# Kernel tuning notes

Hardware: AMD Instinct MI355X
Metric: run time of the kernel (lower is better)

The kernel has to match this reference:

```python
import jax, jax.numpy as jnp
import numpy as np

B, N, C = 64, 1700, 256
E_SP, E_TM = 6400, 10000


def gcn_conv(x, W, b, edge_index, num_nodes):
    """PyG GCNConv (normalize=True, add_self_loops=True) on batched [B,N,C] input,
    gathering/scattering along the node axis (node_dim=-2)."""
    row, col = edge_index[0], edge_index[1]
    loops = jnp.arange(num_nodes, dtype=row.dtype)
    row = jnp.concatenate([row, loops])
    col = jnp.concatenate([col, loops])
    w = jnp.ones(row.shape[0], dtype=x.dtype)
    deg = jax.ops.segment_sum(w, col, num_segments=num_nodes)
    dinv = jnp.where(deg > 0, jax.lax.rsqrt(deg), jnp.zeros_like(deg))
    norm = dinv[row] * dinv[col]                      # [E+N]
    h = x @ W                                         # [B,N,Cout]
    msg = h[:, row, :] * norm[None, :, None]          # gather along joints
    out = jnp.zeros((x.shape[0], num_nodes, W.shape[1]), x.dtype)
    out = out.at[:, col, :].add(msg)                  # scatter-add along joints
    return out + b


def setup_inputs() -> dict:
    key = jax.random.key(0)
    ks = jax.random.split(key, 9)
    s = 1.0 / np.sqrt(C)
    return {
        "x": jax.random.normal(ks[0], (B, N, C), jnp.float32),
        "W1": jax.random.uniform(ks[1], (C, C), jnp.float32, -s, s),
        "b1": jnp.zeros((C,), jnp.float32),
        "W2": jax.random.uniform(ks[2], (C, C), jnp.float32, -s, s),
        "b2": jnp.zeros((C,), jnp.float32),
        "W3": jax.random.uniform(ks[3], (C, C), jnp.float32, -s, s),
        "b3": jnp.zeros((C,), jnp.float32),
        "keypoint_line_without_temporal": jax.random.randint(ks[4], (2, E_SP), 0, N, jnp.int32),
        "keypoint_line_with_temporal": jax.random.randint(ks[5], (2, E_TM), 0, N, jnp.int32),
    }


def reference(x, W1, b1, W2, b2, W3, b3,
              keypoint_line_without_temporal, keypoint_line_with_temporal):
    num_nodes = x.shape[1]
    residual = x  # downsample is None -> identity residual
    out = jax.nn.relu(gcn_conv(x, W1, b1, keypoint_line_without_temporal, num_nodes))
    out = jax.nn.relu(gcn_conv(out, W2, b2, keypoint_line_with_temporal, num_nodes))
    out = gcn_conv(out, W3, b3, keypoint_line_without_temporal, num_nodes)
    return jax.nn.relu(out + residual)
```

## Files before the change

### kernel.cpp

```cpp
#include <hip/hip_runtime.h>

#define NNODES 1700
#define CDIM   256

typedef __attribute__((ext_vector_type(8))) short bf16x8;
typedef __attribute__((ext_vector_type(4))) float f32x4;

__device__ inline float bf2f(unsigned h) { return __uint_as_float(h << 16); }
__device__ inline unsigned short f2bf(float f) {
  unsigned u = __float_as_uint(f);
  u = (u + 0x7FFFu + ((u >> 16) & 1u)) >> 16;
  return (unsigned short)u;
}

__device__ inline void async_copy16(const void* gsrc, void* ldst) {
  __builtin_amdgcn_global_load_lds(
      (const __attribute__((address_space(1))) unsigned int*)gsrc,
      (__attribute__((address_space(3))) unsigned int*)ldst,
      16, 0, 0);
}


__global__ __launch_bounds__(256) void prep1(const float* __restrict__ W1,
                                             const float* __restrict__ W2,
                                             const float* __restrict__ W3,
                                             unsigned short* __restrict__ Wt,
                                             int* __restrict__ zb) {
  int i = blockIdx.x * 256 + threadIdx.x;
  if (i < 4 * NNODES) zb[i] = 0;
  if (i < 3 * 65536) {
    int wsel = i >> 16, e = i & 65535;
    const float* W = wsel == 0 ? W1 : (wsel == 1 ? W2 : W3);
    int k = e >> 8, n = e & 255;
    Wt[(wsel << 16) + n * 256 + k] = f2bf(W[e]);
  }
}

__global__ __launch_bounds__(256) void prep2(const int* __restrict__ esp, int Esp,
                                             const int* __restrict__ etm, int Etm,
                                             int* __restrict__ cnt_sp,
                                             int* __restrict__ cnt_tm) {
  int i = blockIdx.x * 256 + threadIdx.x;
  if (i < Esp) {
    atomicAdd(&cnt_sp[esp[Esp + i]], 1);
  } else {
    int k = i - Esp;
    if (k < Etm) atomicAdd(&cnt_tm[etm[Etm + k]], 1);
  }
}

__global__ __launch_bounds__(1024) void prep3(const int* __restrict__ cnt_sp,
                                              float* __restrict__ dinv_sp,
                                              int* __restrict__ off_sp,
                                              const int* __restrict__ cnt_tm,
                                              float* __restrict__ dinv_tm,
                                              int* __restrict__ off_tm) {
  const int* cnt = blockIdx.x ? cnt_tm : cnt_sp;
  float* dinv = blockIdx.x ? dinv_tm : dinv_sp;
  int* off = blockIdx.x ? off_tm : off_sp;
  __shared__ int s[2048];
  int t = threadIdx.x;
  for (int i = t; i < NNODES; i += 1024) dinv[i] = rsqrtf((float)(cnt[i] + 1));
  for (int i = t; i < 2048; i += 1024) s[i] = (i < NNODES) ? (cnt[i] + 1) : 0;
  for (int d = 1; d < 2048; d <<= 1) {
    __syncthreads();
    int idx = (t + 1) * (d << 1) - 1;
    if (idx < 2048) s[idx] += s[idx - d];
  }
  __syncthreads();
  if (t == 0) s[2047] = 0;
  for (int d = 1024; d >= 1; d >>= 1) {
    __syncthreads();
    int idx = (t + 1) * (d << 1) - 1;
    if (idx < 2048) { int tmp = s[idx - d]; s[idx - d] = s[idx]; s[idx] += tmp; }
  }
  __syncthreads();
  for (int i = t; i <= NNODES; i += 1024) off[i] = s[i];
}

__global__ __launch_bounds__(256) void prep4(
    const int* __restrict__ esp, int Esp, const int* __restrict__ etm, int Etm,
    const float* __restrict__ dinv_sp, const int* __restrict__ off_sp,
    int* __restrict__ cur_sp, int* __restrict__ src_sp, float* __restrict__ wgt_sp,
    const float* __restrict__ dinv_tm, const int* __restrict__ off_tm,
    int* __restrict__ cur_tm, int* __restrict__ src_tm, float* __restrict__ wgt_tm) {
  int i = blockIdx.x * 256 + threadIdx.x;
  const int tot_sp = Esp + NNODES;
  if (i < tot_sp) {
    int s, d;
    if (i < Esp) { s = esp[i]; d = esp[Esp + i]; } else { s = d = i - Esp; }
    float w = dinv_sp[s] * dinv_sp[d];
    int p = atomicAdd(&cur_sp[d], 1);
    int idx = off_sp[d] + p;
    src_sp[idx] = s; wgt_sp[idx] = w;
  } else {
    int k = i - tot_sp;
    if (k < Etm + NNODES) {
      int s, d;
      if (k < Etm) { s = etm[k]; d = etm[Etm + k]; } else { s = d = k - Etm; }
      float w = dinv_tm[s] * dinv_tm[d];
      int p = atomicAdd(&cur_tm[d], 1);
      int idx = off_tm[d] + p;
      src_tm[idx] = s; wgt_tm[idx] = w;
    }
  }
}


template <bool SRCF32>
__global__ __launch_bounds__(256) void agg_kernel(const void* __restrict__ Xp,
                                                  const int* __restrict__ off,
                                                  const int* __restrict__ srcv,
                                                  const float* __restrict__ wv,
                                                  unsigned short* __restrict__ Xa) {
  const int n = blockIdx.x;
  const int b = blockIdx.y * 8 + (threadIdx.x >> 5);
  const int c = (threadIdx.x & 31) * 8;
  const int beg = off[n], end = off[n + 1];
  const size_t base = (size_t)b * NNODES;

  float a0 = 0.f, a1 = 0.f, a2 = 0.f, a3 = 0.f;
  float a4 = 0.f, a5 = 0.f, a6 = 0.f, a7 = 0.f;
  for (int i = beg; i < end; i += 2) {
    int s0 = srcv[i];
    float w0 = wv[i];
    const bool two = (i + 1 < end);
    int i1 = two ? i + 1 : i;
    int s1 = srcv[i1];
    float w1 = two ? wv[i1] : 0.f;
    if (SRCF32) {
      const float* X = (const float*)Xp;
      const float* p0 = X + (base + s0) * CDIM + c;
      const float* p1 = X + (base + s1) * CDIM + c;
      float4 u0 = *(const float4*)p0, u1 = *(const float4*)(p0 + 4);
      float4 v0 = *(const float4*)p1, v1 = *(const float4*)(p1 + 4);
      a0 += w0 * u0.x + w1 * v0.x; a1 += w0 * u0.y + w1 * v0.y;
      a2 += w0 * u0.z + w1 * v0.z; a3 += w0 * u0.w + w1 * v0.w;
      a4 += w0 * u1.x + w1 * v1.x; a5 += w0 * u1.y + w1 * v1.y;
      a6 += w0 * u1.z + w1 * v1.z; a7 += w0 * u1.w + w1 * v1.w;
    } else {
      const unsigned short* X = (const unsigned short*)Xp;
      uint4 u = *(const uint4*)(X + (base + s0) * CDIM + c);
      uint4 v = *(const uint4*)(X + (base + s1) * CDIM + c);
      a0 += w0 * bf2f(u.x & 0xffffu) + w1 * bf2f(v.x & 0xffffu);
      a1 += w0 * bf2f(u.x >> 16)     + w1 * bf2f(v.x >> 16);
      a2 += w0 * bf2f(u.y & 0xffffu) + w1 * bf2f(v.y & 0xffffu);
      a3 += w0 * bf2f(u.y >> 16)     + w1 * bf2f(v.y >> 16);
      a4 += w0 * bf2f(u.z & 0xffffu) + w1 * bf2f(v.z & 0xffffu);
      a5 += w0 * bf2f(u.z >> 16)     + w1 * bf2f(v.z >> 16);
      a6 += w0 * bf2f(u.w & 0xffffu) + w1 * bf2f(v.w & 0xffffu);
      a7 += w0 * bf2f(u.w >> 16)     + w1 * bf2f(v.w >> 16);
    }
  }
  bf16x8 ov;
  ov[0] = (short)f2bf(a0); ov[1] = (short)f2bf(a1);
  ov[2] = (short)f2bf(a2); ov[3] = (short)f2bf(a3);
  ov[4] = (short)f2bf(a4); ov[5] = (short)f2bf(a5);
  ov[6] = (short)f2bf(a6); ov[7] = (short)f2bf(a7);
  *(bf16x8*)(Xa + (base + n) * CDIM + c) = ov;
}


template <int K>
__device__ __forceinline__ void kstep(const unsigned short* __restrict__ asrc,
                                      const unsigned short* __restrict__ bsrc,
                                      unsigned short (&As)[2][128 * 32],
                                      unsigned short (&Bs)[2][64 * 32],
                                      int t, int wm, int wn, int lr, int lk,
                                      f32x4 (&acc)[4][2]) {
  if constexpr (K < 7) {
    asm volatile("s_waitcnt vmcnt(3)" ::: "memory");
  } else {
    asm volatile("s_waitcnt vmcnt(0)" ::: "memory");
  }
  __builtin_amdgcn_s_barrier();
  bf16x8 a[4], b[2];
#pragma unroll
  for (int i = 0; i < 4; i++)
    a[i] = *(const bf16x8*)&As[K & 1][(wm + i * 16 + lr) * 32 + lk];
#pragma unroll
  for (int i = 0; i < 2; i++)
    b[i] = *(const bf16x8*)&Bs[K & 1][(wn + i * 16 + lr) * 32 + lk];
  asm volatile("s_waitcnt lgkmcnt(0)" ::: "memory");
  __builtin_amdgcn_sched_barrier(0);
  __builtin_amdgcn_s_barrier();
  if constexpr (K + 2 < 8) {
    constexpr int S = K + 2;
    async_copy16(asrc + S * 32, &As[S & 1][t * 8]);
    async_copy16(asrc + (size_t)64 * CDIM + S * 32, &As[S & 1][2048 + t * 8]);
    async_copy16(bsrc + S * 32, &Bs[S & 1][t * 8]);
  }
#pragma unroll
  for (int mi = 0; mi < 4; mi++)
#pragma unroll
    for (int ni = 0; ni < 2; ni++)
      acc[mi][ni] = __builtin_amdgcn_mfma_f32_16x16x32_bf16(a[mi], b[ni], acc[mi][ni], 0, 0, 0);
}

template <bool FINAL>
__global__ __launch_bounds__(256, 5) void gemm_t64(const unsigned short* __restrict__ A,
                                                   const unsigned short* __restrict__ Wt,
                                                   const float* __restrict__ bias,
                                                   const float* __restrict__ resid,
                                                   void* __restrict__ outp) {
  __shared__ __align__(16) unsigned short As[2][128 * 32];
  __shared__ __align__(16) unsigned short Bs[2][64 * 32];
  const int t = threadIdx.x;
  const int lane = t & 63;
  const int w = t >> 6;
  const int wm = (w & 1) * 64;
  const int wn = (w >> 1) * 32;
  const int lr = lane & 15;
  const int lk = (lane >> 4) * 8;

  const int chunk = gridDim.x >> 3;
  const int swz = (blockIdx.x & 7) * chunk + (blockIdx.x >> 3);
  const int m0 = (swz >> 2) * 128;
  const int n0 = (swz & 3) * 64;

  const unsigned short* asrc = A + (size_t)(m0 + (t >> 2)) * CDIM + (t & 3) * 8;
  const unsigned short* bsrc = Wt + (size_t)(n0 + (t >> 2)) * CDIM + (t & 3) * 8;

  f32x4 acc[4][2] = {};

#pragma unroll
  for (int s = 0; s < 2; s++) {
    async_copy16(asrc + s * 32, &As[s][t * 8]);
    async_copy16(asrc + (size_t)64 * CDIM + s * 32, &As[s][2048 + t * 8]);
    async_copy16(bsrc + s * 32, &Bs[s][t * 8]);
  }

  kstep<0>(asrc, bsrc, As, Bs, t, wm, wn, lr, lk, acc);
  kstep<1>(asrc, bsrc, As, Bs, t, wm, wn, lr, lk, acc);
  kstep<2>(asrc, bsrc, As, Bs, t, wm, wn, lr, lk, acc);
  kstep<3>(asrc, bsrc, As, Bs, t, wm, wn, lr, lk, acc);
  kstep<4>(asrc, bsrc, As, Bs, t, wm, wn, lr, lk, acc);
  kstep<5>(asrc, bsrc, As, Bs, t, wm, wn, lr, lk, acc);
  kstep<6>(asrc, bsrc, As, Bs, t, wm, wn, lr, lk, acc);
  kstep<7>(asrc, bsrc, As, Bs, t, wm, wn, lr, lk, acc);

  float bv[2];
#pragma unroll
  for (int ni = 0; ni < 2; ni++) bv[ni] = bias[n0 + wn + ni * 16 + lr];
  const int orow = (lane >> 4) * 4;
#pragma unroll
  for (int mi = 0; mi < 4; mi++) {
#pragma unroll
    for (int ni = 0; ni < 2; ni++) {
#pragma unroll
      for (int r = 0; r < 4; r++) {
        const size_t gr = (size_t)(m0 + wm + mi * 16 + orow + r);
        const size_t idx = gr * CDIM + n0 + wn + ni * 16 + lr;
        float v = acc[mi][ni][r] + bv[ni];
        if (FINAL) {
          v += resid[idx];
          ((float*)outp)[idx] = fmaxf(v, 0.f);
        } else {
          ((unsigned short*)outp)[idx] = f2bf(fmaxf(v, 0.f));
        }
      }
    }
  }
}


extern "C" void kernel_launch(void* const* d_in, const int* in_sizes, int n_in,
                              void* d_out, int out_size, void* d_ws, size_t ws_size,
                              hipStream_t stream) {
  const float* x  = (const float*)d_in[0];
  const float* W1 = (const float*)d_in[1];
  const float* b1 = (const float*)d_in[2];
  const float* W2 = (const float*)d_in[3];
  const float* b2 = (const float*)d_in[4];
  const float* W3 = (const float*)d_in[5];
  const float* b3 = (const float*)d_in[6];
  const int* esp = (const int*)d_in[7];
  const int* etm = (const int*)d_in[8];

  const int Esp = in_sizes[7] / 2;
  const int Etm = in_sizes[8] / 2;
  const int B = in_sizes[0] / (NNODES * CDIM);
  const int M = B * NNODES;

  char* ws = (char*)d_ws;
  size_t woff = 0;
  auto alloc = [&](size_t bytes) -> void* {
    void* p = ws + woff;
    woff = (woff + bytes + 255) & ~(size_t)255;
    return p;
  };

  unsigned short* H   = (unsigned short*)alloc((size_t)M * CDIM * 2);
  unsigned short* Act = (unsigned short*)alloc((size_t)M * CDIM * 2);
  unsigned short* Wt  = (unsigned short*)alloc((size_t)3 * CDIM * CDIM * 2);
  int* zero_base = (int*)alloc((size_t)4 * NNODES * sizeof(int));
  int* cnt_sp = zero_base;
  int* cur_sp = zero_base + NNODES;
  int* cnt_tm = zero_base + 2 * NNODES;
  int* cur_tm = zero_base + 3 * NNODES;
  int* off_sp = (int*)alloc((NNODES + 1) * sizeof(int));
  int* off_tm = (int*)alloc((NNODES + 1) * sizeof(int));
  float* dinv_sp = (float*)alloc(NNODES * sizeof(float));
  float* dinv_tm = (float*)alloc(NNODES * sizeof(float));
  int*   src_sp = (int*)alloc((size_t)(Esp + NNODES) * sizeof(int));
  float* wgt_sp = (float*)alloc((size_t)(Esp + NNODES) * sizeof(float));
  int*   src_tm = (int*)alloc((size_t)(Etm + NNODES) * sizeof(int));
  float* wgt_tm = (float*)alloc((size_t)(Etm + NNODES) * sizeof(float));

  prep1<<<(3 * 65536 + 255) / 256, 256, 0, stream>>>(W1, W2, W3, Wt, zero_base);
  prep2<<<(Esp + Etm + 255) / 256, 256, 0, stream>>>(esp, Esp, etm, Etm, cnt_sp, cnt_tm);
  prep3<<<2, 1024, 0, stream>>>(cnt_sp, dinv_sp, off_sp, cnt_tm, dinv_tm, off_tm);
  prep4<<<(Esp + Etm + 2 * NNODES + 255) / 256, 256, 0, stream>>>(
      esp, Esp, etm, Etm, dinv_sp, off_sp, cur_sp, src_sp, wgt_sp,
      dinv_tm, off_tm, cur_tm, src_tm, wgt_tm);

  dim3 agrid(NNODES, B / 8);
  dim3 ggrid(4 * (M / 128));

  agg_kernel<true><<<agrid, 256, 0, stream>>>(x, off_sp, src_sp, wgt_sp, Act);
  gemm_t64<false><<<ggrid, 256, 0, stream>>>(Act, Wt, b1, nullptr, H);
  agg_kernel<false><<<agrid, 256, 0, stream>>>(H, off_tm, src_tm, wgt_tm, Act);
  gemm_t64<false><<<ggrid, 256, 0, stream>>>(Act, Wt + CDIM * CDIM, b2, nullptr, H);
  agg_kernel<false><<<agrid, 256, 0, stream>>>(H, off_sp, src_sp, wgt_sp, Act);
  gemm_t64<true><<<ggrid, 256, 0, stream>>>(Act, Wt + 2 * CDIM * CDIM, b3, x, d_out);
}
```

Before: 437.5 us.

## Split aggregation into per-dtype kernels with finer thread mapping; stage GEMM stores through LDS

The aggregation kernel is split into f32 and bf16 variants where each thread handles 4 channels instead of 8. Blocks cover fewer batches (2 or 4) and use a swizzled 1D grid, which raises parallelism and memory-level concurrency for the gather-heavy step. The non-final GEMM epilogue now stages bf16 results in shared memory and writes 16-byte coalesced rows instead of scattered 2-byte stores. The costs are more blocks, more index loads per byte fetched, and extra barriers in the epilogue.

After: 420.9 us. -3.8%, faster.

```diff
diff --git a/kernel.cpp b/kernel.cpp
--- a/kernel.cpp
+++ b/kernel.cpp
@@ -107,20 +107,21 @@
 }
 
 
-template <bool SRCF32>
-__global__ __launch_bounds__(256) void agg_kernel(const void* __restrict__ Xp,
-                                                  const int* __restrict__ off,
-                                                  const int* __restrict__ srcv,
-                                                  const float* __restrict__ wv,
-                                                  unsigned short* __restrict__ Xa) {
-  const int n = blockIdx.x;
-  const int b = blockIdx.y * 8 + (threadIdx.x >> 5);
-  const int c = (threadIdx.x & 31) * 8;
+__global__ __launch_bounds__(128) void agg_f32(const float* __restrict__ X,
+                                               const int* __restrict__ off,
+                                               const int* __restrict__ srcv,
+                                               const float* __restrict__ wv,
+                                               unsigned short* __restrict__ Xa) {
+  const int perx = gridDim.x >> 3;
+  const int gidx = (blockIdx.x & 7) * perx + (blockIdx.x >> 3);
+  const int g = gidx / NNODES;
+  const int n = gidx - g * NNODES;
+  const int b = g * 2 + (threadIdx.x >> 6);
+  const int c = (threadIdx.x & 63) * 4;
   const int beg = off[n], end = off[n + 1];
   const size_t base = (size_t)b * NNODES;
 
   float a0 = 0.f, a1 = 0.f, a2 = 0.f, a3 = 0.f;
-  float a4 = 0.f, a5 = 0.f, a6 = 0.f, a7 = 0.f;
   for (int i = beg; i < end; i += 2) {
     int s0 = srcv[i];
     float w0 = wv[i];
@@ -128,44 +129,57 @@
     int i1 = two ? i + 1 : i;
     int s1 = srcv[i1];
     float w1 = two ? wv[i1] : 0.f;
-    if (SRCF32) {
-      const float* X = (const float*)Xp;
-      const float* p0 = X + (base + s0) * CDIM + c;
-      const float* p1 = X + (base + s1) * CDIM + c;
-      float4 u0 = *(const float4*)p0, u1 = *(const float4*)(p0 + 4);
-      float4 v0 = *(const float4*)p1, v1 = *(const float4*)(p1 + 4);
-      a0 += w0 * u0.x + w1 * v0.x; a1 += w0 * u0.y + w1 * v0.y;
-      a2 += w0 * u0.z + w1 * v0.z; a3 += w0 * u0.w + w1 * v0.w;
-      a4 += w0 * u1.x + w1 * v1.x; a5 += w0 * u1.y + w1 * v1.y;
-      a6 += w0 * u1.z + w1 * v1.z; a7 += w0 * u1.w + w1 * v1.w;
-    } else {
-      const unsigned short* X = (const unsigned short*)Xp;
-      uint4 u = *(const uint4*)(X + (base + s0) * CDIM + c);
-      uint4 v = *(const uint4*)(X + (base + s1) * CDIM + c);
-      a0 += w0 * bf2f(u.x & 0xffffu) + w1 * bf2f(v.x & 0xffffu);
-      a1 += w0 * bf2f(u.x >> 16)     + w1 * bf2f(v.x >> 16);
-      a2 += w0 * bf2f(u.y & 0xffffu) + w1 * bf2f(v.y & 0xffffu);
-      a3 += w0 * bf2f(u.y >> 16)     + w1 * bf2f(v.y >> 16);
-      a4 += w0 * bf2f(u.z & 0xffffu) + w1 * bf2f(v.z & 0xffffu);
-      a5 += w0 * bf2f(u.z >> 16)     + w1 * bf2f(v.z >> 16);
-      a6 += w0 * bf2f(u.w & 0xffffu) + w1 * bf2f(v.w & 0xffffu);
-      a7 += w0 * bf2f(u.w >> 16)     + w1 * bf2f(v.w >> 16);
-    }
-  }
-  bf16x8 ov;
-  ov[0] = (short)f2bf(a0); ov[1] = (short)f2bf(a1);
-  ov[2] = (short)f2bf(a2); ov[3] = (short)f2bf(a3);
-  ov[4] = (short)f2bf(a4); ov[5] = (short)f2bf(a5);
-  ov[6] = (short)f2bf(a6); ov[7] = (short)f2bf(a7);
-  *(bf16x8*)(Xa + (base + n) * CDIM + c) = ov;
+    float4 u = *(const float4*)(X + (base + s0) * CDIM + c);
+    float4 v = *(const float4*)(X + (base + s1) * CDIM + c);
+    a0 += w0 * u.x + w1 * v.x; a1 += w0 * u.y + w1 * v.y;
+    a2 += w0 * u.z + w1 * v.z; a3 += w0 * u.w + w1 * v.w;
+  }
+  uint2 o;
+  o.x = (unsigned)f2bf(a0) | ((unsigned)f2bf(a1) << 16);
+  o.y = (unsigned)f2bf(a2) | ((unsigned)f2bf(a3) << 16);
+  *(uint2*)(Xa + (base + n) * CDIM + c) = o;
+}
+
+__global__ __launch_bounds__(256) void agg_bf16(const unsigned short* __restrict__ X,
+                                                const int* __restrict__ off,
+                                                const int* __restrict__ srcv,
+                                                const float* __restrict__ wv,
+                                                unsigned short* __restrict__ Xa) {
+  const int perx = gridDim.x >> 3;
+  const int gidx = (blockIdx.x & 7) * perx + (blockIdx.x >> 3);
+  const int g = gidx / NNODES;
+  const int n = gidx - g * NNODES;
+  const int b = g * 4 + (threadIdx.x >> 6);
+  const int c = (threadIdx.x & 63) * 4;
+  const int beg = off[n], end = off[n + 1];
+  const size_t base = (size_t)b * NNODES;
+
+  float a0 = 0.f, a1 = 0.f, a2 = 0.f, a3 = 0.f;
+  for (int i = beg; i < end; i += 2) {
+    int s0 = srcv[i];
+    float w0 = wv[i];
+    const bool two = (i + 1 < end);
+    int i1 = two ? i + 1 : i;
+    int s1 = srcv[i1];
+    float w1 = two ? wv[i1] : 0.f;
+    uint2 u = *(const uint2*)(X + (base + s0) * CDIM + c);
+    uint2 v = *(const uint2*)(X + (base + s1) * CDIM + c);
+    a0 += w0 * bf2f(u.x & 0xffffu) + w1 * bf2f(v.x & 0xffffu);
+    a1 += w0 * bf2f(u.x >> 16)     + w1 * bf2f(v.x >> 16);
+    a2 += w0 * bf2f(u.y & 0xffffu) + w1 * bf2f(v.y & 0xffffu);
+    a3 += w0 * bf2f(u.y >> 16)     + w1 * bf2f(v.y >> 16);
+  }
+  uint2 o;
+  o.x = (unsigned)f2bf(a0) | ((unsigned)f2bf(a1) << 16);
+  o.y = (unsigned)f2bf(a2) | ((unsigned)f2bf(a3) << 16);
+  *(uint2*)(Xa + (base + n) * CDIM + c) = o;
 }
 
 
 template <int K>
 __device__ __forceinline__ void kstep(const unsigned short* __restrict__ asrc,
                                       const unsigned short* __restrict__ bsrc,
-                                      unsigned short (&As)[2][128 * 32],
-                                      unsigned short (&Bs)[2][64 * 32],
+                                      unsigned short* SH,
                                       int t, int wm, int wn, int lr, int lk,
                                       f32x4 (&acc)[4][2]) {
   if constexpr (K < 7) {
@@ -177,18 +191,18 @@
   bf16x8 a[4], b[2];
 #pragma unroll
   for (int i = 0; i < 4; i++)
-    a[i] = *(const bf16x8*)&As[K & 1][(wm + i * 16 + lr) * 32 + lk];
+    a[i] = *(const bf16x8*)&SH[(K & 1) * 4096 + (wm + i * 16 + lr) * 32 + lk];
 #pragma unroll
   for (int i = 0; i < 2; i++)
-    b[i] = *(const bf16x8*)&Bs[K & 1][(wn + i * 16 + lr) * 32 + lk];
+    b[i] = *(const bf16x8*)&SH[8192 + (K & 1) * 2048 + (wn + i * 16 + lr) * 32 + lk];
   asm volatile("s_waitcnt lgkmcnt(0)" ::: "memory");
   __builtin_amdgcn_sched_barrier(0);
   __builtin_amdgcn_s_barrier();
   if constexpr (K + 2 < 8) {
     constexpr int S = K + 2;
-    async_copy16(asrc + S * 32, &As[S & 1][t * 8]);
-    async_copy16(asrc + (size_t)64 * CDIM + S * 32, &As[S & 1][2048 + t * 8]);
-    async_copy16(bsrc + S * 32, &Bs[S & 1][t * 8]);
+    async_copy16(asrc + S * 32, &SH[(S & 1) * 4096 + t * 8]);
+    async_copy16(asrc + (size_t)64 * CDIM + S * 32, &SH[(S & 1) * 4096 + 2048 + t * 8]);
+    async_copy16(bsrc + S * 32, &SH[8192 + (S & 1) * 2048 + t * 8]);
   }
 #pragma unroll
   for (int mi = 0; mi < 4; mi++)
@@ -203,8 +217,7 @@
                                                    const float* __restrict__ bias,
                                                    const float* __restrict__ resid,
                                                    void* __restrict__ outp) {
-  __shared__ __align__(16) unsigned short As[2][128 * 32];
-  __shared__ __align__(16) unsigned short Bs[2][64 * 32];
+  __shared__ __align__(16) unsigned short SH[12288];
   const int t = threadIdx.x;
   const int lane = t & 63;
   const int w = t >> 6;
@@ -225,40 +238,59 @@
 
 #pragma unroll
   for (int s = 0; s < 2; s++) {
-    async_copy16(asrc + s * 32, &As[s][t * 8]);
-    async_copy16(asrc + (size_t)64 * CDIM + s * 32, &As[s][2048 + t * 8]);
-    async_copy16(bsrc + s * 32, &Bs[s][t * 8]);
-  }
-
-  kstep<0>(asrc, bsrc, As, Bs, t, wm, wn, lr, lk, acc);
-  kstep<1>(asrc, bsrc, As, Bs, t, wm, wn, lr, lk, acc);
-  kstep<2>(asrc, bsrc, As, Bs, t, wm, wn, lr, lk, acc);
-  kstep<3>(asrc, bsrc, As, Bs, t, wm, wn, lr, lk, acc);
-  kstep<4>(asrc, bsrc, As, Bs, t, wm, wn, lr, lk, acc);
-  kstep<5>(asrc, bsrc, As, Bs, t, wm, wn, lr, lk, acc);
-  kstep<6>(asrc, bsrc, As, Bs, t, wm, wn, lr, lk, acc);
-  kstep<7>(asrc, bsrc, As, Bs, t, wm, wn, lr, lk, acc);
+    async_copy16(asrc + s * 32, &SH[s * 4096 + t * 8]);
+    async_copy16(asrc + (size_t)64 * CDIM + s * 32, &SH[s * 4096 + 2048 + t * 8]);
+    async_copy16(bsrc + s * 32, &SH[8192 + s * 2048 + t * 8]);
+  }
+
+  kstep<0>(asrc, bsrc, SH, t, wm, wn, lr, lk, acc);
+  kstep<1>(asrc, bsrc, SH, t, wm, wn, lr, lk, acc);
+  kstep<2>(asrc, bsrc, SH, t, wm, wn, lr, lk, acc);
+  kstep<3>(asrc, bsrc, SH, t, wm, wn, lr, lk, acc);
+  kstep<4>(asrc, bsrc, SH, t, wm, wn, lr, lk, acc);
+  kstep<5>(asrc, bsrc, SH, t, wm, wn, lr, lk, acc);
+  kstep<6>(asrc, bsrc, SH, t, wm, wn, lr, lk, acc);
+  kstep<7>(asrc, bsrc, SH, t, wm, wn, lr, lk, acc);
 
   float bv[2];
 #pragma unroll
   for (int ni = 0; ni < 2; ni++) bv[ni] = bias[n0 + wn + ni * 16 + lr];
   const int orow = (lane >> 4) * 4;
-#pragma unroll
-  for (int mi = 0; mi < 4; mi++) {
-#pragma unroll
-    for (int ni = 0; ni < 2; ni++) {
-#pragma unroll
-      for (int r = 0; r < 4; r++) {
-        const size_t gr = (size_t)(m0 + wm + mi * 16 + orow + r);
-        const size_t idx = gr * CDIM + n0 + wn + ni * 16 + lr;
-        float v = acc[mi][ni][r] + bv[ni];
-        if (FINAL) {
-          v += resid[idx];
+
+  if (FINAL) {
+#pragma unroll
+    for (int mi = 0; mi < 4; mi++) {
+#pragma unroll
+      for (int ni = 0; ni < 2; ni++) {
+#pragma unroll
+        for (int r = 0; r < 4; r++) {
+          const size_t gr = (size_t)(m0 + wm + mi * 16 + orow + r);
+          const size_t idx = gr * CDIM + n0 + wn + ni * 16 + lr;
+          float v = acc[mi][ni][r] + bv[ni] + resid[idx];
           ((float*)outp)[idx] = fmaxf(v, 0.f);
-        } else {
-          ((unsigned short*)outp)[idx] = f2bf(fmaxf(v, 0.f));
         }
       }
+    }
+  } else {
+    __syncthreads();
+#pragma unroll
+    for (int mi = 0; mi < 4; mi++)
+#pragma unroll
+      for (int ni = 0; ni < 2; ni++)
+#pragma unroll
+        for (int r = 0; r < 4; r++) {
+          const int row = wm + mi * 16 + orow + r;
+          const int col = wn + ni * 16 + lr;
+          SH[row * 72 + col] = f2bf(fmaxf(acc[mi][ni][r] + bv[ni], 0.f));
+        }
+    __syncthreads();
+    unsigned short* O = (unsigned short*)outp;
+#pragma unroll
+    for (int q = 0; q < 4; q++) {
+      const int cch = q * 256 + t;
+      const int row = cch >> 3, j = cch & 7;
+      bf16x8 v = *(const bf16x8*)&SH[row * 72 + j * 8];
+      *(bf16x8*)(O + (size_t)(m0 + row) * CDIM + n0 + j * 8) = v;
     }
   }
 }
@@ -314,13 +346,14 @@
       esp, Esp, etm, Etm, dinv_sp, off_sp, cur_sp, src_sp, wgt_sp,
       dinv_tm, off_tm, cur_tm, src_tm, wgt_tm);
 
-  dim3 agrid(NNODES, B / 8);
+  dim3 agrid_f(NNODES * (B / 2));
+  dim3 agrid_b(NNODES * (B / 4));
   dim3 ggrid(4 * (M / 128));
 
-  agg_kernel<true><<<agrid, 256, 0, stream>>>(x, off_sp, src_sp, wgt_sp, Act);
+  agg_f32<<<agrid_f, 128, 0, stream>>>(x, off_sp, src_sp, wgt_sp, Act);
   gemm_t64<false><<<ggrid, 256, 0, stream>>>(Act, Wt, b1, nullptr, H);
-  agg_kernel<false><<<agrid, 256, 0, stream>>>(H, off_tm, src_tm, wgt_tm, Act);
+  agg_bf16<<<agrid_b, 256, 0, stream>>>(H, off_tm, src_tm, wgt_tm, Act);
   gemm_t64<false><<<ggrid, 256, 0, stream>>>(Act, Wt + CDIM * CDIM, b2, nullptr, H);
-  agg_kernel<false><<<agrid, 256, 0, stream>>>(H, off_sp, src_sp, wgt_sp, Act);
+  agg_bf16<<<agrid_b, 256, 0, stream>>>(H, off_sp, src_sp, wgt_sp, Act);
   gemm_t64<true><<<ggrid, 256, 0, stream>>>(Act, Wt + 2 * CDIM * CDIM, b3, x, d_out);
 }
```
